# Kernel tuning notes

Measured on AMD Instinct MI355X. Metric: run time of the kernel, lower is better.

## Reference

```python
import jax, jax.numpy as jnp
import numpy as np

# Irreps structure: (multiplicity, component dim 2l+1) for 64x0e + 32x1o + 16x2e
MULTS = (64, 32, 16)
DIMS = (1, 3, 5)
N_NODES = 65536
NUM_TYPES = 64


def setup_inputs() -> dict:
    key = jax.random.key(0)
    k_x, k_idx, k0, k1, k2 = jax.random.split(key, 5)
    dim = sum(m * d for m, d in zip(MULTS, DIMS))  # 240
    x = jax.random.normal(k_x, (N_NODES, dim), dtype=jnp.float32)
    idx = jax.random.randint(k_idx, (N_NODES,), 0, NUM_TYPES)
    W0 = jax.random.normal(k0, (NUM_TYPES, 64, 64), dtype=jnp.float32)
    W1 = jax.random.normal(k1, (NUM_TYPES, 32, 32), dtype=jnp.float32)
    W2 = jax.random.normal(k2, (NUM_TYPES, 16, 16), dtype=jnp.float32)
    return {"x": x, "W0": W0, "W1": W1, "W2": W2, "idx": idx}


def reference(x, W0, W1, W2, idx):
    """Indexed e3nn-style linear: per-node index gathers a weight set; each
    irrep block mixes multiplicity channels (shared across the 2l+1 components)
    with e3nn path normalization 1/sqrt(m_in)."""
    n = x.shape[0]
    outs = []
    off = 0
    for W, m, d in zip((W0, W1, W2), MULTS, DIMS):
        blk = x[:, off:off + m * d].reshape(n, m, d)  # [N, m_in, 2l+1]
        off += m * d
        Wn = W[idx]  # gather per-node weights: [N, m_in, m_out]
        scale = np.float32(1.0 / np.sqrt(m))
        out = jnp.einsum('nio,nid->nod', Wn, blk) * scale  # [N, m_out, 2l+1]
        outs.append(out.reshape(n, m * d))
    return jnp.concatenate(outs, axis=-1)
```

## Files before the change

kernel.cpp:

```cpp
#include <hip/hip_runtime.h>

typedef __attribute__((ext_vector_type(8))) short short8;
typedef __attribute__((ext_vector_type(4))) float floatx4;

#define NTYPES   64
#define ROWS_PB  256
#define THREADS  512
#define NW       8
#define MAXTILES 80
#define WT_STRIDE 5632

__device__ __forceinline__ unsigned short f2bf(float f) {
    union { float f; unsigned u; } v; v.f = f;
    unsigned u = v.u;
    u += 0x7FFFu + ((u >> 16) & 1u);
    return (unsigned short)(u >> 16);
}

__global__ __launch_bounds__(256) void wt_kernel(const float* __restrict__ W0,
                                                 const float* __restrict__ W1,
                                                 const float* __restrict__ W2,
                                                 unsigned short* __restrict__ wt) {
    const int t = blockIdx.x, tid = threadIdx.x;
    unsigned short* dst = wt + (size_t)t * WT_STRIDE;
    const float* w0 = W0 + (size_t)t * 4096;
    for (int e = tid; e < 4096; e += 256) {
        int f = e >> 9, rem = e & 511, rr = rem >> 5, k2 = rem & 31;
        int i = (f & 1) * 32 + k2, o = (f >> 1) * 16 + rr;
        dst[e] = f2bf(w0[i * 64 + o] * 0.125f);
    }
    const float* w1 = W1 + (size_t)t * 1024;
    for (int e = tid; e < 1024; e += 256) {
        int h = e >> 9, rem = e & 511, rr = rem >> 5, k = rem & 31;
        dst[4096 + e] = f2bf(w1[k * 32 + h * 16 + rr] * 0.17677669529663687f);
    }
    const float* w2 = W2 + (size_t)t * 256;
    for (int e = tid; e < 512; e += 256) {
        int rr = e >> 5, k = e & 31;
        dst[5120 + e] = (k < 16) ? f2bf(w2[k * 16 + rr] * 0.25f) : (unsigned short)0;
    }
}

__global__ __launch_bounds__(THREADS, 1) void main_kernel(
    const float* __restrict__ x,
    const int* __restrict__ gidx,
    const unsigned short* __restrict__ wt,
    float* __restrict__ out, int n)
{
    __shared__ __align__(16) unsigned short xrow[ROWS_PB * 240];
    __shared__ int cnts[NTYPES], cur[NTYPES];
    __shared__ unsigned short tlist[ROWS_PB];
    __shared__ unsigned short ttype[MAXTILES], tstt[MAXTILES], trws[MAXTILES];
    __shared__ int ntiles;

    const int b = blockIdx.x, tid = threadIdx.x;
    const int nbase = b * ROWS_PB;
    const int nvalid = min(ROWS_PB, n - nbase);

#pragma unroll
    for (int t = 0; t < 30; ++t) {
        int e = t * THREADS + tid;
        int row = e / 60, c4 = e - row * 60;
        if (row < nvalid) {
            float4 f = *(const float4*)(x + (size_t)(nbase + row) * 240 + c4 * 4);
            ushort4 u;
            u.x = f2bf(f.x); u.y = f2bf(f.y); u.z = f2bf(f.z); u.w = f2bf(f.w);
            *(ushort4*)(xrow + row * 240 + c4 * 4) = u;
        }
    }

    if (tid < NTYPES) cnts[tid] = 0;
    __syncthreads();
    int myty = -1;
    if (tid < nvalid) { myty = gidx[nbase + tid]; atomicAdd(&cnts[myty], 1); }
    __syncthreads();
    if (tid == 0) {
        int acc = 0, ntl = 0;
        for (int t = 0; t < NTYPES; ++t) {
            int c = cnts[t];
            cur[t] = acc;
            for (int s = 0; s < c; s += 16) {
                ttype[ntl] = (unsigned short)t;
                tstt[ntl]  = (unsigned short)(acc + s);
                trws[ntl]  = (unsigned short)min(16, c - s);
                ++ntl;
            }
            acc += c;
        }
        ntiles = ntl;
    }
    __syncthreads();
    if (tid < nvalid) { int p = atomicAdd(&cur[myty], 1); tlist[p] = (unsigned short)tid; }
    __syncthreads();

    const int wv = tid >> 6, ln = tid & 63;
    const int r = ln & 15, q4 = ln >> 4;
    const int NT = ntiles;

    for (int ti = wv; ti < NT; ti += NW) {
        const int ty = ttype[ti], st = tstt[ti], rows = trws[ti];
        const int lr = tlist[st + min(r, rows - 1)];
        const unsigned short* xr = xrow + lr * 240;

        short8 a00 = *(const short8*)(xr + q4 * 8);
        short8 a01 = *(const short8*)(xr + 32 + q4 * 8);
        short8 a1[3];
#pragma unroll
        for (int d = 0; d < 3; ++d)
#pragma unroll
            for (int j = 0; j < 8; ++j)
                ((unsigned short*)&a1[d])[j] = xr[64 + (q4 * 8 + j) * 3 + d];
        short8 a2[5];
#pragma unroll
        for (int d = 0; d < 5; ++d) {
            a2[d] = short8{0, 0, 0, 0, 0, 0, 0, 0};
            if (q4 < 2)
#pragma unroll
                for (int j = 0; j < 8; ++j)
                    ((unsigned short*)&a2[d])[j] = xr[160 + (q4 * 8 + j) * 5 + d];
        }

        size_t ob[4]; bool vr[4];
#pragma unroll
        for (int rr = 0; rr < 4; ++rr) {
            int rowi = q4 * 4 + rr;
            vr[rr] = rowi < rows;
            int lrr = __shfl(lr, rowi);
            ob[rr] = (size_t)(nbase + lrr) * 240;
        }

        const unsigned short* wb = wt + (size_t)ty * WT_STRIDE;

#pragma unroll
        for (int nt = 0; nt < 4; ++nt) {
            short8 b0 = *(const short8*)(wb + (nt * 2) * 512 + r * 32 + q4 * 8);
            short8 b1 = *(const short8*)(wb + (nt * 2 + 1) * 512 + r * 32 + q4 * 8);
            floatx4 ac = {0.f, 0.f, 0.f, 0.f};
            ac = __builtin_amdgcn_mfma_f32_16x16x32_bf16(a00, b0, ac, 0, 0, 0);
            ac = __builtin_amdgcn_mfma_f32_16x16x32_bf16(a01, b1, ac, 0, 0, 0);
#pragma unroll
            for (int rr = 0; rr < 4; ++rr)
                if (vr[rr]) out[ob[rr] + nt * 16 + r] = ac[rr];
        }

        {
            short8 c0 = *(const short8*)(wb + 4096 + r * 32 + q4 * 8);
            short8 c1 = *(const short8*)(wb + 4096 + 512 + r * 32 + q4 * 8);
#pragma unroll
            for (int d = 0; d < 3; ++d) {
                floatx4 ac = {0.f, 0.f, 0.f, 0.f};
                ac = __builtin_amdgcn_mfma_f32_16x16x32_bf16(a1[d], c0, ac, 0, 0, 0);
#pragma unroll
                for (int rr = 0; rr < 4; ++rr)
                    if (vr[rr]) out[ob[rr] + 64 + r * 3 + d] = ac[rr];
                floatx4 ac2 = {0.f, 0.f, 0.f, 0.f};
                ac2 = __builtin_amdgcn_mfma_f32_16x16x32_bf16(a1[d], c1, ac2, 0, 0, 0);
#pragma unroll
                for (int rr = 0; rr < 4; ++rr)
                    if (vr[rr]) out[ob[rr] + 64 + (16 + r) * 3 + d] = ac2[rr];
            }
        }

        {
            short8 c2 = *(const short8*)(wb + 5120 + r * 32 + q4 * 8);
#pragma unroll
            for (int d = 0; d < 5; ++d) {
                floatx4 ac = {0.f, 0.f, 0.f, 0.f};
                ac = __builtin_amdgcn_mfma_f32_16x16x32_bf16(a2[d], c2, ac, 0, 0, 0);
#pragma unroll
                for (int rr = 0; rr < 4; ++rr)
                    if (vr[rr]) out[ob[rr] + 160 + r * 5 + d] = ac[rr];
            }
        }
    }
}

extern "C" void kernel_launch(void* const* d_in, const int* in_sizes, int n_in,
                              void* d_out, int out_size, void* d_ws, size_t ws_size,
                              hipStream_t stream) {
    const float* x  = (const float*)d_in[0];
    const float* W0 = (const float*)d_in[1];
    const float* W1 = (const float*)d_in[2];
    const float* W2 = (const float*)d_in[3];
    const int*   idx = (const int*)d_in[4];
    float* out = (float*)d_out;
    const int n = in_sizes[4];
    unsigned short* wt = (unsigned short*)d_ws;

    wt_kernel  <<<NTYPES, 256, 0, stream>>>(W0, W1, W2, wt);
    main_kernel<<<(n + ROWS_PB - 1) / ROWS_PB, THREADS, 0, stream>>>(x, idx, wt, out, n);
}
```

Measured before the change: 161.0 us.

## Globally sort nodes by type and transpose MFMA tiles for vectorized stores

```diff
diff --git a/kernel.cpp b/kernel.cpp
--- a/kernel.cpp
+++ b/kernel.cpp
@@ -3,12 +3,11 @@
 typedef __attribute__((ext_vector_type(8))) short short8;
 typedef __attribute__((ext_vector_type(4))) float floatx4;
 
-#define NTYPES   64
-#define ROWS_PB  256
-#define THREADS  512
-#define NW       8
-#define MAXTILES 80
+#define NTYPES    64
 #define WT_STRIDE 5632
+#define ROWS_PB   64
+#define THREADS   256
+#define ROW_U     248
 
 __device__ __forceinline__ unsigned short f2bf(float f) {
     union { float f; unsigned u; } v; v.f = f;
@@ -21,155 +20,225 @@
                                                  const float* __restrict__ W1,
                                                  const float* __restrict__ W2,
                                                  unsigned short* __restrict__ wt) {
+    __shared__ float ws0[4096];
+    __shared__ float ws1[1024];
+    __shared__ float ws2[256];
     const int t = blockIdx.x, tid = threadIdx.x;
+    const float4* s0 = (const float4*)(W0 + (size_t)t * 4096);
+#pragma unroll
+    for (int j = 0; j < 4; ++j) ((float4*)ws0)[j * 256 + tid] = s0[j * 256 + tid];
+    ((float4*)ws1)[tid] = ((const float4*)(W1 + (size_t)t * 1024))[tid];
+    if (tid < 64) ((float4*)ws2)[tid] = ((const float4*)(W2 + (size_t)t * 256))[tid];
+    __syncthreads();
     unsigned short* dst = wt + (size_t)t * WT_STRIDE;
-    const float* w0 = W0 + (size_t)t * 4096;
     for (int e = tid; e < 4096; e += 256) {
         int f = e >> 9, rem = e & 511, rr = rem >> 5, k2 = rem & 31;
         int i = (f & 1) * 32 + k2, o = (f >> 1) * 16 + rr;
-        dst[e] = f2bf(w0[i * 64 + o] * 0.125f);
-    }
-    const float* w1 = W1 + (size_t)t * 1024;
+        dst[e] = f2bf(ws0[i * 64 + o] * 0.125f);
+    }
     for (int e = tid; e < 1024; e += 256) {
         int h = e >> 9, rem = e & 511, rr = rem >> 5, k = rem & 31;
-        dst[4096 + e] = f2bf(w1[k * 32 + h * 16 + rr] * 0.17677669529663687f);
-    }
-    const float* w2 = W2 + (size_t)t * 256;
+        dst[4096 + e] = f2bf(ws1[k * 32 + h * 16 + rr] * 0.17677669529663687f);
+    }
     for (int e = tid; e < 512; e += 256) {
         int rr = e >> 5, k = e & 31;
-        dst[5120 + e] = (k < 16) ? f2bf(w2[k * 16 + rr] * 0.25f) : (unsigned short)0;
-    }
-}
-
-__global__ __launch_bounds__(THREADS, 1) void main_kernel(
+        dst[5120 + e] = (k < 16) ? f2bf(ws2[k * 16 + rr] * 0.25f) : (unsigned short)0;
+    }
+}
+
+__global__ __launch_bounds__(256) void hist_kernel(const int* __restrict__ idx,
+                                                   int* __restrict__ bh, int n) {
+    __shared__ int c[NTYPES];
+    const int b = blockIdx.x, tid = threadIdx.x;
+    if (tid < NTYPES) c[tid] = 0;
+    __syncthreads();
+    int g = b * 256 + tid;
+    if (g < n) atomicAdd(&c[idx[g]], 1);
+    __syncthreads();
+    if (tid < NTYPES) bh[b * NTYPES + tid] = c[tid];
+}
+
+__global__ __launch_bounds__(64) void scan_kernel(const int* __restrict__ bh,
+                                                  int* __restrict__ obh,
+                                                  int* __restrict__ tbase, int nb) {
+    __shared__ int tot[NTYPES], pre[NTYPES];
+    const int t = threadIdx.x;
+    int run = 0;
+    for (int b = 0; b < nb; ++b) {
+        int v = bh[b * NTYPES + t];
+        obh[b * NTYPES + t] = run;
+        run += v;
+    }
+    tot[t] = run;
+    __syncthreads();
+    if (t == 0) {
+        int a = 0;
+        for (int u = 0; u < NTYPES; ++u) { pre[u] = a; a += tot[u]; }
+    }
+    __syncthreads();
+    tbase[t] = pre[t];
+}
+
+__global__ __launch_bounds__(256) void scatter_kernel(const int* __restrict__ idx,
+                                                      const int* __restrict__ obh,
+                                                      const int* __restrict__ tbase,
+                                                      int* __restrict__ psort, int n) {
+    __shared__ int cur[NTYPES], off[NTYPES];
+    const int b = blockIdx.x, tid = threadIdx.x;
+    if (tid < NTYPES) { cur[tid] = 0; off[tid] = tbase[tid] + obh[b * NTYPES + tid]; }
+    __syncthreads();
+    int g = b * 256 + tid;
+    if (g < n) {
+        int ty = idx[g];
+        int rk = atomicAdd(&cur[ty], 1);
+        psort[off[ty] + rk] = g | (ty << 24);
+    }
+}
+
+__global__ __launch_bounds__(THREADS, 4) void main_kernel(
     const float* __restrict__ x,
-    const int* __restrict__ gidx,
+    const int* __restrict__ psort,
     const unsigned short* __restrict__ wt,
     float* __restrict__ out, int n)
 {
-    __shared__ __align__(16) unsigned short xrow[ROWS_PB * 240];
-    __shared__ int cnts[NTYPES], cur[NTYPES];
-    __shared__ unsigned short tlist[ROWS_PB];
-    __shared__ unsigned short ttype[MAXTILES], tstt[MAXTILES], trws[MAXTILES];
+    __shared__ __align__(16) unsigned short xrow[ROWS_PB * ROW_U];
+    __shared__ int pls[ROWS_PB];
+    __shared__ int tinfo[ROWS_PB];
     __shared__ int ntiles;
 
     const int b = blockIdx.x, tid = threadIdx.x;
     const int nbase = b * ROWS_PB;
-    const int nvalid = min(ROWS_PB, n - nbase);
-
-#pragma unroll
-    for (int t = 0; t < 30; ++t) {
-        int e = t * THREADS + tid;
+    const int nv = min(ROWS_PB, n - nbase);
+    const int wv = tid >> 6, ln = tid & 63;
+
+    if (tid < ROWS_PB) pls[tid] = (nbase + tid < n) ? psort[nbase + tid] : 0;
+    __syncthreads();
+
+    if (wv == 0) {
+        int v = (ln < nv) ? (pls[ln] >> 24) : -1;
+        int pv = __shfl_up(v, 1);
+        bool bnd = (ln < nv) && (ln == 0 || v != pv);
+        unsigned long long bm = __ballot(bnd);
+        if (ln == 0) {
+            int ntl = 0;
+            unsigned long long m = bm;
+            while (m) {
+                unsigned long long m2 = m & (m - 1);
+                int s = (int)__builtin_ctzll(m);
+                int e = m2 ? (int)__builtin_ctzll(m2) : nv;
+                int t = pls[s] >> 24;
+                for (int q = s; q < e; q += 16)
+                    tinfo[ntl++] = (t << 16) | (q << 8) | min(16, e - q);
+                m = m2;
+            }
+            ntiles = ntl;
+        }
+    }
+
+#pragma unroll
+    for (int it = 0; it < 15; ++it) {
+        int e = it * THREADS + tid;
         int row = e / 60, c4 = e - row * 60;
-        if (row < nvalid) {
-            float4 f = *(const float4*)(x + (size_t)(nbase + row) * 240 + c4 * 4);
-            ushort4 u;
-            u.x = f2bf(f.x); u.y = f2bf(f.y); u.z = f2bf(f.z); u.w = f2bf(f.w);
-            *(ushort4*)(xrow + row * 240 + c4 * 4) = u;
-        }
-    }
-
-    if (tid < NTYPES) cnts[tid] = 0;
-    __syncthreads();
-    int myty = -1;
-    if (tid < nvalid) { myty = gidx[nbase + tid]; atomicAdd(&cnts[myty], 1); }
-    __syncthreads();
-    if (tid == 0) {
-        int acc = 0, ntl = 0;
-        for (int t = 0; t < NTYPES; ++t) {
-            int c = cnts[t];
-            cur[t] = acc;
-            for (int s = 0; s < c; s += 16) {
-                ttype[ntl] = (unsigned short)t;
-                tstt[ntl]  = (unsigned short)(acc + s);
-                trws[ntl]  = (unsigned short)min(16, c - s);
-                ++ntl;
-            }
-            acc += c;
-        }
-        ntiles = ntl;
-    }
-    __syncthreads();
-    if (tid < nvalid) { int p = atomicAdd(&cur[myty], 1); tlist[p] = (unsigned short)tid; }
-    __syncthreads();
-
-    const int wv = tid >> 6, ln = tid & 63;
+        if (row < nv) {
+            int node = pls[row] & 0xFFFFFF;
+            float4 f = *(const float4*)(x + (size_t)node * 240 + c4 * 4);
+            unsigned short qq[4] = {f2bf(f.x), f2bf(f.y), f2bf(f.z), f2bf(f.w)};
+            unsigned short* xr = xrow + row * ROW_U;
+            if (c4 < 16) {
+                *(ushort4*)(xr + c4 * 4) = ushort4{qq[0], qq[1], qq[2], qq[3]};
+            } else if (c4 < 40) {
+                int t0 = c4 * 4 - 64;
+                int i = t0 / 3, d = t0 - i * 3;
+#pragma unroll
+                for (int j = 0; j < 4; ++j) {
+                    xr[64 + d * 32 + i] = qq[j];
+                    if (++d == 3) { d = 0; ++i; }
+                }
+            } else {
+                int t0 = c4 * 4 - 160;
+                int i = t0 / 5, d = t0 - i * 5;
+#pragma unroll
+                for (int j = 0; j < 4; ++j) {
+                    xr[160 + d * 16 + i] = qq[j];
+                    if (++d == 5) { d = 0; ++i; }
+                }
+            }
+        }
+    }
+    __syncthreads();
+
     const int r = ln & 15, q4 = ln >> 4;
     const int NT = ntiles;
 
-    for (int ti = wv; ti < NT; ti += NW) {
-        const int ty = ttype[ti], st = tstt[ti], rows = trws[ti];
-        const int lr = tlist[st + min(r, rows - 1)];
-        const unsigned short* xr = xrow + lr * 240;
-
-        short8 a00 = *(const short8*)(xr + q4 * 8);
-        short8 a01 = *(const short8*)(xr + 32 + q4 * 8);
-        short8 a1[3];
-#pragma unroll
-        for (int d = 0; d < 3; ++d)
-#pragma unroll
-            for (int j = 0; j < 8; ++j)
-                ((unsigned short*)&a1[d])[j] = xr[64 + (q4 * 8 + j) * 3 + d];
-        short8 a2[5];
-#pragma unroll
-        for (int d = 0; d < 5; ++d) {
-            a2[d] = short8{0, 0, 0, 0, 0, 0, 0, 0};
-            if (q4 < 2)
-#pragma unroll
-                for (int j = 0; j < 8; ++j)
-                    ((unsigned short*)&a2[d])[j] = xr[160 + (q4 * 8 + j) * 5 + d];
-        }
-
-        size_t ob[4]; bool vr[4];
-#pragma unroll
-        for (int rr = 0; rr < 4; ++rr) {
-            int rowi = q4 * 4 + rr;
-            vr[rr] = rowi < rows;
-            int lrr = __shfl(lr, rowi);
-            ob[rr] = (size_t)(nbase + lrr) * 240;
-        }
-
+    for (int ti = wv; ti < NT; ti += (THREADS / 64)) {
+        const int info = tinfo[ti];
+        const int ty = info >> 16, s0 = (info >> 8) & 0xFF, rows = info & 0xFF;
+        const int lrow = s0 + min(r, rows - 1);
+        const unsigned short* xr = xrow + lrow * ROW_U;
         const unsigned short* wb = wt + (size_t)ty * WT_STRIDE;
+        const bool vst = (r < rows);
+        const int gnode = vst ? (pls[s0 + r] & 0xFFFFFF) : 0;
+        float* op = out + (size_t)gnode * 240;
+
+        short8 bx0 = *(const short8*)(xr + q4 * 8);
+        short8 bx1 = *(const short8*)(xr + 32 + q4 * 8);
 
 #pragma unroll
         for (int nt = 0; nt < 4; ++nt) {
-            short8 b0 = *(const short8*)(wb + (nt * 2) * 512 + r * 32 + q4 * 8);
-            short8 b1 = *(const short8*)(wb + (nt * 2 + 1) * 512 + r * 32 + q4 * 8);
+            short8 wa = *(const short8*)(wb + (nt * 2) * 512 + r * 32 + q4 * 8);
+            short8 wc = *(const short8*)(wb + (nt * 2 + 1) * 512 + r * 32 + q4 * 8);
             floatx4 ac = {0.f, 0.f, 0.f, 0.f};
-            ac = __builtin_amdgcn_mfma_f32_16x16x32_bf16(a00, b0, ac, 0, 0, 0);
-            ac = __builtin_amdgcn_mfma_f32_16x16x32_bf16(a01, b1, ac, 0, 0, 0);
-#pragma unroll
-            for (int rr = 0; rr < 4; ++rr)
-                if (vr[rr]) out[ob[rr] + nt * 16 + r] = ac[rr];
+            ac = __builtin_amdgcn_mfma_f32_16x16x32_bf16(wa, bx0, ac, 0, 0, 0);
+            ac = __builtin_amdgcn_mfma_f32_16x16x32_bf16(wc, bx1, ac, 0, 0, 0);
+            if (vst) *(floatx4*)(op + nt * 16 + q4 * 4) = ac;
         }
 
         {
-            short8 c0 = *(const short8*)(wb + 4096 + r * 32 + q4 * 8);
-            short8 c1 = *(const short8*)(wb + 4096 + 512 + r * 32 + q4 * 8);
+            short8 wc0 = *(const short8*)(wb + 4096 + r * 32 + q4 * 8);
+            short8 wc1 = *(const short8*)(wb + 4096 + 512 + r * 32 + q4 * 8);
+            floatx4 a1[2][3];
 #pragma unroll
             for (int d = 0; d < 3; ++d) {
-                floatx4 ac = {0.f, 0.f, 0.f, 0.f};
-                ac = __builtin_amdgcn_mfma_f32_16x16x32_bf16(a1[d], c0, ac, 0, 0, 0);
-#pragma unroll
-                for (int rr = 0; rr < 4; ++rr)
-                    if (vr[rr]) out[ob[rr] + 64 + r * 3 + d] = ac[rr];
-                floatx4 ac2 = {0.f, 0.f, 0.f, 0.f};
-                ac2 = __builtin_amdgcn_mfma_f32_16x16x32_bf16(a1[d], c1, ac2, 0, 0, 0);
-#pragma unroll
-                for (int rr = 0; rr < 4; ++rr)
-                    if (vr[rr]) out[ob[rr] + 64 + (16 + r) * 3 + d] = ac2[rr];
+                short8 bx = *(const short8*)(xr + 64 + d * 32 + q4 * 8);
+                floatx4 z = {0.f, 0.f, 0.f, 0.f};
+                a1[0][d] = __builtin_amdgcn_mfma_f32_16x16x32_bf16(wc0, bx, z, 0, 0, 0);
+                a1[1][d] = __builtin_amdgcn_mfma_f32_16x16x32_bf16(wc1, bx, z, 0, 0, 0);
+            }
+            if (vst) {
+#pragma unroll
+                for (int h = 0; h < 2; ++h) {
+                    float* o1 = op + 64 + (h * 16 + q4 * 4) * 3;
+                    floatx4 v0 = {a1[h][0][0], a1[h][1][0], a1[h][2][0], a1[h][0][1]};
+                    floatx4 v1 = {a1[h][1][1], a1[h][2][1], a1[h][0][2], a1[h][1][2]};
+                    floatx4 v2 = {a1[h][2][2], a1[h][0][3], a1[h][1][3], a1[h][2][3]};
+                    *(floatx4*)(o1)     = v0;
+                    *(floatx4*)(o1 + 4) = v1;
+                    *(floatx4*)(o1 + 8) = v2;
+                }
             }
         }
 
         {
-            short8 c2 = *(const short8*)(wb + 5120 + r * 32 + q4 * 8);
+            short8 wc2 = *(const short8*)(wb + 5120 + r * 32 + q4 * 8);
+            floatx4 a2[5];
 #pragma unroll
             for (int d = 0; d < 5; ++d) {
-                floatx4 ac = {0.f, 0.f, 0.f, 0.f};
-                ac = __builtin_amdgcn_mfma_f32_16x16x32_bf16(a2[d], c2, ac, 0, 0, 0);
-#pragma unroll
-                for (int rr = 0; rr < 4; ++rr)
-                    if (vr[rr]) out[ob[rr] + 160 + r * 5 + d] = ac[rr];
+                short8 bx = *(const short8*)(xr + 160 + d * 16 + (q4 & 1) * 8);
+                floatx4 z = {0.f, 0.f, 0.f, 0.f};
+                a2[d] = __builtin_amdgcn_mfma_f32_16x16x32_bf16(wc2, bx, z, 0, 0, 0);
+            }
+            if (vst) {
+                float* o2 = op + 160 + q4 * 20;
+                floatx4 v0 = {a2[0][0], a2[1][0], a2[2][0], a2[3][0]};
+                floatx4 v1 = {a2[4][0], a2[0][1], a2[1][1], a2[2][1]};
+                floatx4 v2 = {a2[3][1], a2[4][1], a2[0][2], a2[1][2]};
+                floatx4 v3 = {a2[2][2], a2[3][2], a2[4][2], a2[0][3]};
+                floatx4 v4 = {a2[1][3], a2[2][3], a2[3][3], a2[4][3]};
+                *(floatx4*)(o2)      = v0;
+                *(floatx4*)(o2 + 4)  = v1;
+                *(floatx4*)(o2 + 8)  = v2;
+                *(floatx4*)(o2 + 12) = v3;
+                *(floatx4*)(o2 + 16) = v4;
             }
         }
     }
@@ -185,8 +254,19 @@
     const int*   idx = (const int*)d_in[4];
     float* out = (float*)d_out;
     const int n = in_sizes[4];
-    unsigned short* wt = (unsigned short*)d_ws;
-
-    wt_kernel  <<<NTYPES, 256, 0, stream>>>(W0, W1, W2, wt);
-    main_kernel<<<(n + ROWS_PB - 1) / ROWS_PB, THREADS, 0, stream>>>(x, idx, wt, out, n);
-}
+    const int nb = (n + 255) / 256;
+
+    char* ws = (char*)d_ws;
+    unsigned short* wt = (unsigned short*)ws;
+    size_t off = (size_t)NTYPES * WT_STRIDE * 2;
+    int* psort = (int*)(ws + off); off += (size_t)n * 4;
+    int* bh    = (int*)(ws + off); off += (size_t)nb * NTYPES * 4;
+    int* obh   = (int*)(ws + off); off += (size_t)nb * NTYPES * 4;
+    int* tbase = (int*)(ws + off);
+
+    wt_kernel     <<<NTYPES, 256, 0, stream>>>(W0, W1, W2, wt);
+    hist_kernel   <<<nb, 256, 0, stream>>>(idx, bh, n);
+    scan_kernel   <<<1, 64, 0, stream>>>(bh, obh, tbase, nb);
+    scatter_kernel<<<nb, 256, 0, stream>>>(idx, obh, tbase, psort, n);
+    main_kernel   <<<(n + ROWS_PB - 1) / ROWS_PB, THREADS, 0, stream>>>(x, psort, wt, out, n);
+}
```

Result: slower. 200.5 us (+24.5%).
